# Performance work log

Hardware: AMD Instinct MI355X
Metric: run time of the kernel (lower is better)

## Reference

```python
import jax, jax.numpy as jnp
import numpy as np

B, L, C, H, FF = 2, 2048, 1024, 16, 4096
HD = C // H
SCALE = HD ** -0.5
EPS = 1e-5


def _ln(x, g, b):
    m = jnp.mean(x, axis=-1, keepdims=True)
    v = jnp.mean((x - m) ** 2, axis=-1, keepdims=True)
    return (x - m) * jax.lax.rsqrt(v + EPS) * g + b


def setup_inputs() -> dict:
    key = jax.random.key(0)
    ks = jax.random.split(key, 12)
    s = lambda fan_in: 1.0 / np.sqrt(fan_in)
    return {
        "x": jax.random.normal(ks[0], (B, L, C), jnp.float32),
        "freq_diff": jax.random.normal(ks[1], (B, L), jnp.float32),
        "qkv_w": jax.random.normal(ks[2], (C, 3 * C), jnp.float32) * s(C),
        "qkv_b": jnp.zeros((3 * C,), jnp.float32),
        "fp_w1": jax.random.normal(ks[3], (1, C), jnp.float32),
        "fp_b1": jnp.zeros((C,), jnp.float32),
        "fp_ln_g": jnp.ones((C,), jnp.float32),
        "fp_ln_b": jnp.zeros((C,), jnp.float32),
        "fp_w2": jax.random.normal(ks[4], (C, C), jnp.float32) * s(C),
        "fp_b2": jnp.zeros((C,), jnp.float32),
        "wq_w": jax.random.normal(ks[5], (HD, HD), jnp.float32) * s(HD),
        "wq_b": jnp.zeros((HD,), jnp.float32),
        "wk_w": jax.random.normal(ks[6], (HD, HD), jnp.float32) * s(HD),
        "wk_b": jnp.zeros((HD,), jnp.float32),
        "out_w": jax.random.normal(ks[7], (C, C), jnp.float32) * s(C),
        "out_b": jnp.zeros((C,), jnp.float32),
        "n1_g": jnp.ones((C,), jnp.float32),
        "n1_b": jnp.zeros((C,), jnp.float32),
        "n2_g": jnp.ones((C,), jnp.float32),
        "n2_b": jnp.zeros((C,), jnp.float32),
        "mlp_w1": jax.random.normal(ks[8], (C, FF), jnp.float32) * s(C),
        "mlp_b1": jnp.zeros((FF,), jnp.float32),
        "mlp_w2": jax.random.normal(ks[9], (FF, C), jnp.float32) * s(FF),
        "mlp_b2": jnp.zeros((C,), jnp.float32),
        "freq_scale": jnp.ones((1,), jnp.float32),
    }


def reference(x, freq_diff, qkv_w, qkv_b, fp_w1, fp_b1, fp_ln_g, fp_ln_b,
              fp_w2, fp_b2, wq_w, wq_b, wk_w, wk_b, out_w, out_b,
              n1_g, n1_b, n2_g, n2_b, mlp_w1, mlp_b1, mlp_w2, mlp_b2,
              freq_scale):
    shortcut = x
    xn = _ln(x, n1_g, n1_b)
    qkv = (xn @ qkv_w + qkv_b).reshape(B, L, 3, H, HD)
    qkv = jnp.transpose(qkv, (2, 0, 3, 1, 4))  # [3,B,H,L,HD]
    q, k, v = qkv[0], qkv[1], qkv[2]

    # frequency bias: MLP on scalar freq_diff -> per-head bias vectors
    fb = freq_diff[..., None] @ fp_w1 + fp_b1          # [B,L,C]
    fb = jax.nn.gelu(_ln(fb, fp_ln_g, fp_ln_b), approximate=False)
    fb = fb @ fp_w2 + fp_b2                            # [B,L,C]
    fb = jnp.transpose(fb.reshape(B, L, H, HD), (0, 2, 1, 3))  # [B,H,L,HD]
    qb = fb @ wq_w + wq_b
    kb = fb @ wk_w + wk_b
    freq_attn_bias = jnp.einsum('bhqd,bhkd->bhqk', qb, kb)

    attn = jnp.einsum('bhqd,bhkd->bhqk', q, k) * SCALE
    attn = attn + freq_scale[0] * freq_attn_bias
    attn = jax.nn.softmax(attn, axis=-1)
    o = jnp.einsum('bhqk,bhkd->bhqd', attn, v)
    o = jnp.transpose(o, (0, 2, 1, 3)).reshape(B, L, C)
    x = shortcut + (o @ out_w + out_b)

    xn2 = _ln(x, n2_g, n2_b)
    h = jax.nn.gelu(xn2 @ mlp_w1 + mlp_b1, approximate=False)
    x = x + (h @ mlp_w2 + mlp_b2)
    return x
```

## Files before the change

### kernel.cpp

```cpp
#include <hip/hip_runtime.h>
#include <math.h>


typedef __bf16 bf16;
typedef float f32x4 __attribute__((ext_vector_type(4)));
typedef bf16 bf16x8 __attribute__((ext_vector_type(8)));
typedef bf16 bf16x4 __attribute__((ext_vector_type(4)));

#define DEVINL __device__ __forceinline__

#define LOG2E 1.4426950408889634f

DEVINL float fast_exp2(float x) { return __builtin_amdgcn_exp2f(x); }

DEVINL void async_load16(const void* g, void* l) {
  __builtin_amdgcn_global_load_lds(
      (const __attribute__((address_space(1))) unsigned int*)g,
      (__attribute__((address_space(3))) unsigned int*)l, 16, 0, 0);
}

DEVINL f32x4 mfma16(bf16x8 a, bf16x8 b, f32x4 c) {
  return __builtin_amdgcn_mfma_f32_16x16x32_bf16(a, b, c, 0, 0, 0);
}

DEVINL float gelu_exact(float v) {
  return 0.5f * v * (1.0f + erff(v * 0.70710678118654752f));
}

DEVINL void hard_barrier() {
  asm volatile("" ::: "memory");
  __builtin_amdgcn_s_barrier();
  asm volatile("" ::: "memory");
}

DEVINL void block_reduce2(float& a, float& b, float* red, int tid) {
#pragma unroll
  for (int off = 32; off >= 1; off >>= 1) {
    a += __shfl_xor(a, off);
    b += __shfl_xor(b, off);
  }
  int w = tid >> 6;
  if ((tid & 63) == 0) { red[2 * w] = a; red[2 * w + 1] = b; }
  __syncthreads();
  a = red[0] + red[2] + red[4] + red[6];
  b = red[1] + red[3] + red[5] + red[7];
  __syncthreads();
}

__global__ __launch_bounds__(256) void transpose_cast(
    const float* __restrict__ W, bf16* __restrict__ Wt, int K, int N) {
  __shared__ float tile[32][33];
  int n0 = blockIdx.x * 32, k0 = blockIdx.y * 32;
  int tx = threadIdx.x & 31, ty = threadIdx.x >> 5;
#pragma unroll
  for (int r = 0; r < 4; ++r)
    tile[ty + r * 8][tx] = W[(size_t)(k0 + ty + r * 8) * N + n0 + tx];
  __syncthreads();
#pragma unroll
  for (int r = 0; r < 4; ++r)
    Wt[(size_t)(n0 + ty + r * 8) * K + k0 + tx] = (bf16)tile[tx][ty + r * 8];
}

__global__ __launch_bounds__(256) void prec_qk(
    const float* __restrict__ fp_w2, const float* __restrict__ fp_b2,
    const float* __restrict__ wq_w, const float* __restrict__ wq_b,
    const float* __restrict__ wk_w, const float* __restrict__ wk_b,
    bf16* __restrict__ wqk2t, float* __restrict__ bqk) {
  __shared__ float Wl[64 * 64];
  __shared__ float Al[64 * 128];
  const int id = blockIdx.x;
  const int sel = id >> 7, h = (id >> 3) & 15, ck = id & 7;
  const int t = threadIdx.x;
  const float* wsel = sel ? wk_w : wq_w;
#pragma unroll
  for (int i = 0; i < 4; ++i)
    ((float4*)Wl)[i * 256 + t] = ((const float4*)wsel)[i * 256 + t];
  const int c0 = ck * 128, off = h * 64;
#pragma unroll
  for (int it = 0; it < 8; ++it) {
    int idx = it * 256 + t;
    int rr = idx >> 4, c4 = idx & 15;
    float4 v = *(const float4*)(fp_w2 + (size_t)(c0 + rr) * 1024 + off + c4 * 4);
    float vv[4] = {v.x, v.y, v.z, v.w};
#pragma unroll
    for (int k = 0; k < 4; ++k) {
      int i2 = c4 * 4 + k;
      Al[i2 * 128 + (rr ^ (i2 & 31))] = vv[k];
    }
  }
  __syncthreads();
  const int cr = t & 127, jh = (t >> 7) * 32;
  float acc[32];
#pragma unroll
  for (int j = 0; j < 32; ++j) acc[j] = 0.f;
  for (int i = 0; i < 64; ++i) {
    float a = Al[i * 128 + (cr ^ (i & 31))];
    const float4* wrow = (const float4*)(Wl + i * 64 + jh);
#pragma unroll
    for (int j4 = 0; j4 < 8; ++j4) {
      float4 wv = wrow[j4];
      acc[j4 * 4 + 0] += a * wv.x;
      acc[j4 * 4 + 1] += a * wv.y;
      acc[j4 * 4 + 2] += a * wv.z;
      acc[j4 * 4 + 3] += a * wv.w;
    }
  }
  const int nbase = sel * 1024 + off + jh;
#pragma unroll
  for (int j = 0; j < 32; ++j)
    wqk2t[(size_t)(nbase + j) * 1024 + c0 + cr] = (bf16)acc[j];
  if (ck == 0 && t < 64) {
    float s = 0.f;
    for (int i = 0; i < 64; ++i) s += fp_b2[off + i] * Wl[i * 64 + t];
    bqk[sel * 1024 + off + t] = s + (sel ? wk_b[t] : wq_b[t]);
  }
}

__global__ __launch_bounds__(256) void ln1_kernel(
    const float* __restrict__ x, const float* __restrict__ fd,
    const float* __restrict__ g1, const float* __restrict__ b1,
    const float* __restrict__ fw1, const float* __restrict__ fb1,
    const float* __restrict__ flg, const float* __restrict__ flb,
    bf16* __restrict__ xn, bf16* __restrict__ gout) {
  __shared__ float red[8];
  int tok = blockIdx.x, t = threadIdx.x;
  float4 xv = ((const float4*)(x + (size_t)tok * 1024))[t];
  float s = xv.x + xv.y + xv.z + xv.w;
  float ss = xv.x * xv.x + xv.y * xv.y + xv.z * xv.z + xv.w * xv.w;
  block_reduce2(s, ss, red, t);
  float mean = s * (1.0f / 1024.0f);
  float rsig = rsqrtf(ss * (1.0f / 1024.0f) - mean * mean + 1e-5f);
  float4 g4 = ((const float4*)g1)[t], b4 = ((const float4*)b1)[t];
  bf16x4 o;
  o[0] = (bf16)((xv.x - mean) * rsig * g4.x + b4.x);
  o[1] = (bf16)((xv.y - mean) * rsig * g4.y + b4.y);
  o[2] = (bf16)((xv.z - mean) * rsig * g4.z + b4.z);
  o[3] = (bf16)((xv.w - mean) * rsig * g4.w + b4.w);
  ((bf16x4*)xn)[(size_t)tok * 256 + t] = o;

  float dv = fd[tok];
  float4 w4 = ((const float4*)fw1)[t], c4 = ((const float4*)fb1)[t];
  float f0 = dv * w4.x + c4.x, f1 = dv * w4.y + c4.y;
  float f2 = dv * w4.z + c4.z, f3 = dv * w4.w + c4.w;
  s = f0 + f1 + f2 + f3;
  ss = f0 * f0 + f1 * f1 + f2 * f2 + f3 * f3;
  block_reduce2(s, ss, red, t);
  mean = s * (1.0f / 1024.0f);
  rsig = rsqrtf(ss * (1.0f / 1024.0f) - mean * mean + 1e-5f);
  float4 lg = ((const float4*)flg)[t], lb = ((const float4*)flb)[t];
  bf16x4 q;
  q[0] = (bf16)gelu_exact((f0 - mean) * rsig * lg.x + lb.x);
  q[1] = (bf16)gelu_exact((f1 - mean) * rsig * lg.y + lb.y);
  q[2] = (bf16)gelu_exact((f2 - mean) * rsig * lg.z + lb.z);
  q[3] = (bf16)gelu_exact((f3 - mean) * rsig * lg.w + lb.w);
  ((bf16x4*)gout)[(size_t)tok * 256 + t] = q;
}

__global__ __launch_bounds__(256) void ln_kernel(
    const float* __restrict__ xin, const float* __restrict__ g,
    const float* __restrict__ b, bf16* __restrict__ xout) {
  __shared__ float red[8];
  int tok = blockIdx.x, t = threadIdx.x;
  float4 xv = ((const float4*)(xin + (size_t)tok * 1024))[t];
  float s = xv.x + xv.y + xv.z + xv.w;
  float ss = xv.x * xv.x + xv.y * xv.y + xv.z * xv.z + xv.w * xv.w;
  block_reduce2(s, ss, red, t);
  float mean = s * (1.0f / 1024.0f);
  float rsig = rsqrtf(ss * (1.0f / 1024.0f) - mean * mean + 1e-5f);
  float4 g4 = ((const float4*)g)[t], b4 = ((const float4*)b)[t];
  bf16x4 o;
  o[0] = (bf16)((xv.x - mean) * rsig * g4.x + b4.x);
  o[1] = (bf16)((xv.y - mean) * rsig * g4.y + b4.y);
  o[2] = (bf16)((xv.z - mean) * rsig * g4.z + b4.z);
  o[3] = (bf16)((xv.w - mean) * rsig * g4.w + b4.w);
  ((bf16x4*)xout)[(size_t)tok * 256 + t] = o;
}

#define PHASE(MH, NH, LA, LB, STAGE_STMT, WAIT_STMT)                          \
  do {                                                                        \
    if (LA) {                                                                 \
      _Pragma("unroll") for (int ml = 0; ml < 4; ++ml) {                      \
        _Pragma("unroll") for (int ks = 0; ks < 2; ++ks) {                    \
          const int rr = ml * 16 + lm;                                        \
          const int cc = (((ks * 4 + quad) ^ (lm & 7)) << 3);                 \
          af[ml][ks] = *(const bf16x8*)&As[bsel][MH][wm][rr][cc];             \
        }                                                                     \
      }                                                                       \
    }                                                                         \
    if (LB) {                                                                 \
      _Pragma("unroll") for (int nl = 0; nl < 2; ++nl) {                      \
        _Pragma("unroll") for (int ks = 0; ks < 2; ++ks) {                    \
          const int rr = nl * 16 + lm;                                        \
          const int cc = (((ks * 4 + quad) ^ (lm & 7)) << 3);                 \
          bfr[nl][ks] = *(const bf16x8*)&Bs[bsel][NH][wn][rr][cc];            \
        }                                                                     \
      }                                                                       \
    }                                                                         \
    STAGE_STMT;                                                               \
    hard_barrier();                                                           \
    __builtin_amdgcn_s_setprio(1);                                            \
    _Pragma("unroll") for (int ks = 0; ks < 2; ++ks) {                        \
      _Pragma("unroll") for (int ml = 0; ml < 4; ++ml) {                      \
        _Pragma("unroll") for (int nl = 0; nl < 2; ++nl) {                    \
          acc[(MH)*4 + ml][(NH)*2 + nl] = mfma16(                             \
              af[ml][ks], bfr[nl][ks], acc[(MH)*4 + ml][(NH)*2 + nl]);        \
        }                                                                     \
      }                                                                       \
    }                                                                         \
    __builtin_amdgcn_s_setprio(0);                                            \
    WAIT_STMT;                                                                \
    hard_barrier();                                                           \
  } while (0)

template <class Epi>
__global__ __launch_bounds__(512, 2) void gemm256(
    const bf16* __restrict__ A, const bf16* __restrict__ Bt,
    int lda, int ldb, int K, int kstride, int nbx, int nblk, int rowoffz,
    Epi epi) {
  __shared__ __align__(16) bf16 As[2][2][2][64][64];
  __shared__ __align__(16) bf16 Bs[2][2][4][32][64];

  const int tid = threadIdx.x;
  const int lane = tid & 63, w = tid >> 6;
  const int quad = lane >> 4, lm = lane & 15;
  const int wm = w >> 2, wn = w & 3;

  const int kz = blockIdx.x / nblk;
  const int bid = blockIdx.x - kz * nblk;
  const int swz = (nblk & 7) ? bid : ((bid & 7) * (nblk >> 3) + (bid >> 3));
  const int tm = swz / nbx, tn = swz - tm * nbx;
  const int m0 = tm << 8, n0 = tn << 8;
  const int rowoff = kz * rowoffz;
  A += (size_t)kz * kstride;
  Bt += (size_t)kz * kstride;

  const bf16* Abase = A + (size_t)m0 * lda;
  const bf16* Bbase = Bt + (size_t)n0 * ldb;

  auto stageA = [&](int b, int mh, int kt) {
#pragma unroll
    for (int j = 0; j < 2; ++j) {
      const int q = (w * 2 + j) * 64 + lane;
      const int wm2 = q >> 9, rr = (q >> 3) & 63, c = q & 7;
      async_load16(Abase + (size_t)(wm2 * 128 + mh * 64 + rr) * lda +
                       (size_t)kt * 64 + ((c ^ (rr & 7)) << 3),
                   (char*)&As[b][mh][0][0][0] + (w * 2 + j) * 1024);
    }
  };
  auto stageB = [&](int b, int nh, int kt) {
#pragma unroll
    for (int j = 0; j < 2; ++j) {
      const int q = (w * 2 + j) * 64 + lane;
      const int wn4 = q >> 8, rr = (q >> 3) & 31, c = q & 7;
      async_load16(Bbase + (size_t)(wn4 * 64 + nh * 32 + rr) * ldb +
                       (size_t)kt * 64 + ((c ^ (rr & 7)) << 3),
                   (char*)&Bs[b][nh][0][0][0] + (w * 2 + j) * 1024);
    }
  };

  f32x4 acc[8][4];
#pragma unroll
  for (int i = 0; i < 8; ++i)
#pragma unroll
    for (int j = 0; j < 4; ++j) {
      acc[i][j][0] = 0.f; acc[i][j][1] = 0.f;
      acc[i][j][2] = 0.f; acc[i][j][3] = 0.f;
    }
  bf16x8 af[4][2], bfr[2][2];

  stageA(0, 0, 0);
  stageB(0, 1, 0);
  stageA(0, 1, 0);
  stageB(0, 0, 0);
  stageA(1, 0, 1);
  stageB(1, 1, 1);
  asm volatile("s_waitcnt vmcnt(4)" ::: "memory");
  hard_barrier();

  const int nt = K >> 6;
  int bsel = 0;
  for (int t = 0; t < nt; ++t, bsel ^= 1) {
    PHASE(0, 0, 1, 1, { if (t + 1 < nt) stageA(bsel ^ 1, 1, t + 1); }, {});
    PHASE(0, 1, 0, 1, { if (t + 1 < nt) stageB(bsel ^ 1, 0, t + 1); }, {});
    PHASE(1, 1, 1, 0, { if (t + 2 < nt) stageA(bsel, 0, t + 2); }, {});
    PHASE(1, 0, 0, 1, { if (t + 2 < nt) stageB(bsel, 1, t + 2); },
          {
            if (t + 2 < nt) {
              asm volatile("s_waitcnt vmcnt(4)" ::: "memory");
            } else if (t + 1 < nt) {
              asm volatile("s_waitcnt vmcnt(0)" ::: "memory");
            }
          });
  }

#pragma unroll
  for (int mi = 0; mi < 8; ++mi)
#pragma unroll
    for (int ni = 0; ni < 4; ++ni)
      epi(rowoff + m0 + wm * 128 + mi * 16 + quad * 4,
          n0 + wn * 64 + ni * 16 + lm, acc[mi][ni]);
}

template <class Epi>
__global__ __launch_bounds__(256) void gemm_bf16_k(
    const bf16* __restrict__ A, const bf16* __restrict__ Bt,
    int M, int N, int K, Epi epi) {
  __shared__ bf16 As[2][128 * 32];
  __shared__ bf16 Bs[2][128 * 32];
  const int tid = threadIdx.x;
  const int lane = tid & 63, w = tid >> 6;
  const int quad = lane >> 4, lm = lane & 15;
  const int wm = w >> 1, wn = w & 1;
  const int m0 = blockIdx.y * 128, n0 = blockIdx.x * 128;

  f32x4 acc[4][4];
#pragma unroll
  for (int i = 0; i < 4; ++i)
#pragma unroll
    for (int j = 0; j < 4; ++j) {
      acc[i][j][0] = 0.f; acc[i][j][1] = 0.f; acc[i][j][2] = 0.f; acc[i][j][3] = 0.f;
    }

  const bf16* Ag = A + (size_t)m0 * K;
  const bf16* Bg = Bt + (size_t)n0 * K;

  auto stage = [&](int k0, int buf) {
#pragma unroll
    for (int i = 0; i < 2; ++i) {
      int ch = i * 256 + tid, r = ch >> 2, c = ch & 3;
      async_load16(Ag + (size_t)r * K + k0 + c * 8,
                   (char*)As[buf] + (i * 256 + w * 64) * 16);
      async_load16(Bg + (size_t)r * K + k0 + c * 8,
                   (char*)Bs[buf] + (i * 256 + w * 64) * 16);
    }
  };

  stage(0, 0);
  const int nk = K >> 5;
  for (int ki = 0; ki < nk; ++ki) {
    __syncthreads();
    if (ki + 1 < nk) stage((ki + 1) << 5, (ki + 1) & 1);
    const bf16* Ac = As[ki & 1];
    const bf16* Bc = Bs[ki & 1];
    bf16x8 af[4], bfv[4];
#pragma unroll
    for (int mi = 0; mi < 4; ++mi)
      af[mi] = *(const bf16x8*)(Ac + (wm * 64 + mi * 16 + lm) * 32 + quad * 8);
#pragma unroll
    for (int ni = 0; ni < 4; ++ni)
      bfv[ni] = *(const bf16x8*)(Bc + (wn * 64 + ni * 16 + lm) * 32 + quad * 8);
#pragma unroll
    for (int mi = 0; mi < 4; ++mi)
#pragma unroll
      for (int ni = 0; ni < 4; ++ni)
        acc[mi][ni] = mfma16(af[mi], bfv[ni], acc[mi][ni]);
  }

#pragma unroll
  for (int mi = 0; mi < 4; ++mi)
#pragma unroll
    for (int ni = 0; ni < 4; ++ni)
      epi(m0 + wm * 64 + mi * 16 + quad * 4, n0 + wn * 64 + ni * 16 + lm, acc[mi][ni]);
}

__global__ __launch_bounds__(256) void reduce_mlp2(
    const float* __restrict__ part, float* __restrict__ out) {
  size_t i = (size_t)blockIdx.x * 256 + threadIdx.x;
  const float4* p = (const float4*)part;
  float4 o = ((const float4*)out)[i];
  const size_t S = (size_t)4096 * 256;
  float4 a = p[i], b = p[i + S], c = p[i + 2 * S], d = p[i + 3 * S];
  o.x += a.x + b.x + c.x + d.x;
  o.y += a.y + b.y + c.y + d.y;
  o.z += a.z + b.z + c.z + d.z;
  o.w += a.w + b.w + c.w + d.w;
  ((float4*)out)[i] = o;
}

struct EpiQKV {
  const float* __restrict__ bias;
  bf16 *Qc, *Kc, *Vt;
  DEVINL void operator()(int row, int col, f32x4 v) const {
    int b = row >> 11, l = row & 2047;
    float bia = bias[col];
    if (col < 1024) {
      int h = col >> 6, d = col & 63;
      bf16* p = Qc + (size_t)(((b << 4) + h) * 2048 + l) * 128 + d;
#pragma unroll
      for (int r = 0; r < 4; ++r) p[r * 128] = (bf16)((v[r] + bia) * (0.125f * LOG2E));
    } else if (col < 2048) {
      int c2 = col - 1024, h = c2 >> 6, d = c2 & 63;
      bf16* p = Kc + (size_t)(((b << 4) + h) * 2048 + l) * 128 + d;
#pragma unroll
      for (int r = 0; r < 4; ++r) p[r * 128] = (bf16)(v[r] + bia);
    } else {
      int c2 = col - 2048, h = c2 >> 6, d = c2 & 63;
      bf16x4 pk;
#pragma unroll
      for (int r = 0; r < 4; ++r) pk[r] = (bf16)(v[r] + bia);
      *(bf16x4*)(Vt + (size_t)(((b << 4) + h) * 64 + d) * 2048 + l) = pk;
    }
  }
};

struct EpiQBKB {
  const float* __restrict__ bias;
  const float* __restrict__ fs;
  bf16 *Qc, *Kc;
  DEVINL void operator()(int row, int col, f32x4 v) const {
    int b = row >> 11, l = row & 2047;
    float bia = bias[col];
    if (col < 1024) {
      int h = col >> 6, d = col & 63;
      float sc = fs[0] * LOG2E;
      bf16* p = Qc + (size_t)(((b << 4) + h) * 2048 + l) * 128 + 64 + d;
#pragma unroll
      for (int r = 0; r < 4; ++r) p[r * 128] = (bf16)((v[r] + bia) * sc);
    } else {
      int c2 = col - 1024, h = c2 >> 6, d = c2 & 63;
      bf16* p = Kc + (size_t)(((b << 4) + h) * 2048 + l) * 128 + 64 + d;
#pragma unroll
      for (int r = 0; r < 4; ++r) p[r * 128] = (bf16)(v[r] + bia);
    }
  }
};

struct EpiOut {
  const float* __restrict__ bias;
  const float* __restrict__ x;
  const float* __restrict__ b2;
  float* x1;
  float* out0;
  DEVINL void operator()(int row, int col, f32x4 v) const {
    float bia = bias[col];
    float b2v = b2[col];
#pragma unroll
    for (int r = 0; r < 4; ++r) {
      size_t idx = (size_t)(row + r) * 1024 + col;
      float xv = x[idx] + v[r] + bia;
      x1[idx] = xv;
      out0[idx] = xv + b2v;
    }
  }
};

struct EpiMLP1 {
  const float* __restrict__ bias;
  bf16* hbf;
  DEVINL void operator()(int row, int col, f32x4 v) const {
    float bia = bias[col];
#pragma unroll
    for (int r = 0; r < 4; ++r)
      hbf[(size_t)(row + r) * 4096 + col] = (bf16)gelu_exact(v[r] + bia);
  }
};

struct EpiPart {
  float* part;
  DEVINL void operator()(int row, int col, f32x4 v) const {
#pragma unroll
    for (int r = 0; r < 4; ++r)
      part[(size_t)(row + r) * 1024 + col] = v[r];
  }
};

__global__ __launch_bounds__(512, 4) void flash_kernel(
    const bf16* __restrict__ Qc, const bf16* __restrict__ Kcp,
    const bf16* __restrict__ Vt, bf16* __restrict__ Obf) {
  __shared__ bf16 KsA[64 * 128];
  __shared__ bf16 KsB[64 * 128];
  __shared__ bf16 VsA[64 * 64];
  __shared__ bf16 VsB[64 * 64];
  __shared__ bf16 Ps[128 * 64];

  const int tid = threadIdx.x, lane = tid & 63, w = tid >> 6;
  const int quad = lane >> 4, lm = lane & 15;
  const int id = blockIdx.x;
  const int bh = id & 31, qt = id >> 5;
  const int b = bh >> 4, h = bh & 15;

  const bf16* Qg = Qc + ((size_t)bh * 2048 + qt * 128) * 128;
#pragma unroll
  for (int i = 0; i < 4; ++i) {
    int ch = i * 512 + tid, r = ch >> 4, cs = ch & 15, c = cs ^ (r & 7);
    char* dst = (i < 2) ? (char*)KsA + (i * 512 + w * 64) * 16
                        : (char*)KsB + ((i - 2) * 512 + w * 64) * 16;
    async_load16(Qg + (size_t)r * 128 + c * 8, dst);
  }
  __syncthreads();
  const int qr = w * 16 + lm;
  bf16x8 qf[4];
  {
    const bf16* base = (w < 4) ? KsA : KsB;
    int rr = qr & 63;
#pragma unroll
    for (int ks = 0; ks < 4; ++ks) {
      int pos = (ks * 4 + quad) ^ (lm & 7);
      qf[ks] = *(const bf16x8*)(base + rr * 128 + pos * 8);
    }
  }
  __syncthreads();

  float m_run = -3.0e38f, l_run = 0.f;
  f32x4 o_acc[4];
#pragma unroll
  for (int nf = 0; nf < 4; ++nf) {
    o_acc[nf][0] = 0.f; o_acc[nf][1] = 0.f; o_acc[nf][2] = 0.f; o_acc[nf][3] = 0.f;
  }

  const bf16* Kg0 = Kcp + (size_t)bh * 2048 * 128;
  const bf16* Vg0 = Vt + (size_t)bh * 64 * 2048;

  auto stage = [&](int kv, bf16* Kdst, bf16* Vdst) {
    const bf16* Kg = Kg0 + (size_t)kv * 64 * 128;
#pragma unroll
    for (int i = 0; i < 2; ++i) {
      int ch = i * 512 + tid, key = ch >> 4, c = (ch & 15) ^ (key & 7);
      async_load16(Kg + (size_t)key * 128 + c * 8,
                   (char*)Kdst + (i * 512 + w * 64) * 16);
    }
    {
      int d = tid >> 3, c = (tid & 7) ^ (d & 7);
      async_load16(Vg0 + (size_t)d * 2048 + kv * 64 + c * 8,
                   (char*)Vdst + (w * 64) * 16);
    }
  };

  stage(0, KsA, VsA);

  for (int kv = 0; kv < 32; ++kv) {
    const bf16* Kcur = (kv & 1) ? KsB : KsA;
    const bf16* Vcur = (kv & 1) ? VsB : VsA;
    __syncthreads();
    if (kv + 1 < 32)
      stage(kv + 1, (kv & 1) ? KsA : KsB, (kv & 1) ? VsA : VsB);

    f32x4 sa[4];
#pragma unroll
    for (int nk = 0; nk < 4; ++nk) {
      sa[nk][0] = 0.f; sa[nk][1] = 0.f; sa[nk][2] = 0.f; sa[nk][3] = 0.f;
    }
#pragma unroll
    for (int ks = 0; ks < 4; ++ks) {
      bf16x8 ak[4];
#pragma unroll
      for (int nk = 0; nk < 4; ++nk) {
        int key = nk * 16 + lm;
        int pos = (ks * 4 + quad) ^ (key & 7);
        ak[nk] = *(const bf16x8*)(Kcur + key * 128 + pos * 8);
      }
#pragma unroll
      for (int nk = 0; nk < 4; ++nk)
        sa[nk] = mfma16(ak[nk], qf[ks], sa[nk]);
    }

    float mx = sa[0][0];
#pragma unroll
    for (int nk = 0; nk < 4; ++nk)
#pragma unroll
      for (int rg = 0; rg < 4; ++rg) mx = fmaxf(mx, sa[nk][rg]);
    mx = fmaxf(mx, __shfl_xor(mx, 16));
    mx = fmaxf(mx, __shfl_xor(mx, 32));
    float mnew = fmaxf(m_run, mx);
    float alpha = fast_exp2(m_run - mnew);
    m_run = mnew;
    float rs = 0.f;
#pragma unroll
    for (int nk = 0; nk < 4; ++nk)
#pragma unroll
      for (int rg = 0; rg < 4; ++rg) {
        float pv = fast_exp2(sa[nk][rg] - mnew);
        sa[nk][rg] = pv;
        rs += pv;
      }
    rs += __shfl_xor(rs, 16);
    rs += __shfl_xor(rs, 32);
    l_run = l_run * alpha + rs;
#pragma unroll
    for (int nf = 0; nf < 4; ++nf) {
      o_acc[nf][0] *= alpha; o_acc[nf][1] *= alpha;
      o_acc[nf][2] *= alpha; o_acc[nf][3] *= alpha;
    }

#pragma unroll
    for (int nk = 0; nk < 4; ++nk) {
      int c16 = 2 * nk + (quad >> 1);
      int cs = c16 ^ (lm & 7);
      bf16x4 pk;
      pk[0] = (bf16)sa[nk][0]; pk[1] = (bf16)sa[nk][1];
      pk[2] = (bf16)sa[nk][2]; pk[3] = (bf16)sa[nk][3];
      *(bf16x4*)(Ps + qr * 64 + cs * 8 + (quad & 1) * 4) = pk;
    }

#pragma unroll
    for (int ks = 0; ks < 2; ++ks) {
      bf16x8 pa, vb[4];
      {
        int cs = (ks * 4 + quad) ^ (lm & 7);
        pa = *(const bf16x8*)(Ps + qr * 64 + cs * 8);
      }
#pragma unroll
      for (int nf = 0; nf < 4; ++nf) {
        int d = nf * 16 + lm;
        int cs = (ks * 4 + quad) ^ (d & 7);
        vb[nf] = *(const bf16x8*)(Vcur + d * 64 + cs * 8);
      }
#pragma unroll
      for (int nf = 0; nf < 4; ++nf)
        o_acc[nf] = mfma16(vb[nf], pa, o_acc[nf]);
    }
  }

  float inv = 1.0f / l_run;
  int l = qt * 128 + qr;
#pragma unroll
  for (int nf = 0; nf < 4; ++nf) {
    bf16x4 ov;
#pragma unroll
    for (int rg = 0; rg < 4; ++rg) ov[rg] = (bf16)(o_acc[nf][rg] * inv);
    int d = h * 64 + nf * 16 + quad * 4;
    *(bf16x4*)(Obf + ((size_t)b * 2048 + l) * 1024 + d) = ov;
  }
}

extern "C" void kernel_launch(void* const* d_in, const int* in_sizes, int n_in,
                              void* d_out, int out_size, void* d_ws, size_t ws_size,
                              hipStream_t stream) {
  (void)in_sizes; (void)n_in; (void)out_size; (void)ws_size;
  const float* x      = (const float*)d_in[0];
  const float* fd     = (const float*)d_in[1];
  const float* qkv_w  = (const float*)d_in[2];
  const float* qkv_b  = (const float*)d_in[3];
  const float* fp_w1  = (const float*)d_in[4];
  const float* fp_b1  = (const float*)d_in[5];
  const float* fp_ln_g= (const float*)d_in[6];
  const float* fp_ln_b= (const float*)d_in[7];
  const float* fp_w2  = (const float*)d_in[8];
  const float* fp_b2  = (const float*)d_in[9];
  const float* wq_w   = (const float*)d_in[10];
  const float* wq_b   = (const float*)d_in[11];
  const float* wk_w   = (const float*)d_in[12];
  const float* wk_b   = (const float*)d_in[13];
  const float* out_w  = (const float*)d_in[14];
  const float* out_b  = (const float*)d_in[15];
  const float* n1_g   = (const float*)d_in[16];
  const float* n1_b   = (const float*)d_in[17];
  const float* n2_g   = (const float*)d_in[18];
  const float* n2_b   = (const float*)d_in[19];
  const float* mlp_w1 = (const float*)d_in[20];
  const float* mlp_b1 = (const float*)d_in[21];
  const float* mlp_w2 = (const float*)d_in[22];
  const float* mlp_b2 = (const float*)d_in[23];
  const float* fscale = (const float*)d_in[24];
  float* out = (float*)d_out;

  char* p = (char*)d_ws;
  auto take = [&](size_t n) { char* r = p; p += (n + 255) & ~(size_t)255; return r; };
  bf16* xn_bf  = (bf16*)take((size_t)4096 * 1024 * 2);
  bf16* g_bf   = (bf16*)take((size_t)4096 * 1024 * 2);
  bf16* Qc     = (bf16*)take((size_t)32 * 2048 * 128 * 2);
  bf16* Kc     = (bf16*)take((size_t)32 * 2048 * 128 * 2);
  bf16* Vt     = (bf16*)take((size_t)32 * 64 * 2048 * 2);
  bf16* o_bf   = (bf16*)take((size_t)4096 * 1024 * 2);
  float* x1    = (float*)take((size_t)4096 * 1024 * 4);
  bf16* ln2_bf = (bf16*)take((size_t)4096 * 1024 * 2);
  bf16* h_bf   = (bf16*)take((size_t)4096 * 4096 * 2);
  bf16* qkv_wt = (bf16*)take((size_t)3072 * 1024 * 2);
  bf16* out_wt = (bf16*)take((size_t)1024 * 1024 * 2);
  bf16* w1t    = (bf16*)take((size_t)4096 * 1024 * 2);
  bf16* w2t    = (bf16*)take((size_t)1024 * 4096 * 2);
  bf16* wqk2t  = (bf16*)take((size_t)2048 * 1024 * 2);
  float* bqk   = (float*)take((size_t)2048 * 4);

  float* part = (float*)xn_bf;

  dim3 b256(256), b512(512);

  transpose_cast<<<dim3(3072 / 32, 1024 / 32), b256, 0, stream>>>(qkv_w, qkv_wt, 1024, 3072);
  transpose_cast<<<dim3(1024 / 32, 1024 / 32), b256, 0, stream>>>(out_w, out_wt, 1024, 1024);
  transpose_cast<<<dim3(4096 / 32, 1024 / 32), b256, 0, stream>>>(mlp_w1, w1t, 1024, 4096);
  transpose_cast<<<dim3(1024 / 32, 4096 / 32), b256, 0, stream>>>(mlp_w2, w2t, 4096, 1024);
  prec_qk<<<dim3(256), b256, 0, stream>>>(fp_w2, fp_b2, wq_w, wq_b, wk_w, wk_b, wqk2t, bqk);

  ln1_kernel<<<dim3(4096), b256, 0, stream>>>(x, fd, n1_g, n1_b, fp_w1, fp_b1,
                                              fp_ln_g, fp_ln_b, xn_bf, g_bf);

  gemm256<<<dim3(192), b512, 0, stream>>>(xn_bf, qkv_wt, 1024, 1024, 1024, 0,
                                          12, 192, 0, EpiQKV{qkv_b, Qc, Kc, Vt});
  gemm256<<<dim3(128), b512, 0, stream>>>(g_bf, wqk2t, 1024, 1024, 1024, 0,
                                          8, 128, 0, EpiQBKB{bqk, fscale, Qc, Kc});
  flash_kernel<<<dim3(512), dim3(512), 0, stream>>>(Qc, Kc, Vt, o_bf);

  gemm_bf16_k<<<dim3(8, 32), b256, 0, stream>>>(o_bf, out_wt, 4096, 1024, 1024,
                                                EpiOut{out_b, x, mlp_b2, x1, out});
  ln_kernel<<<dim3(4096), b256, 0, stream>>>(x1, n2_g, n2_b, ln2_bf);
  gemm256<<<dim3(256), b512, 0, stream>>>(ln2_bf, w1t, 1024, 1024, 1024, 0,
                                          16, 256, 0, EpiMLP1{mlp_b1, h_bf});
  gemm256<<<dim3(256), b512, 0, stream>>>(h_bf, w2t, 4096, 4096, 1024, 1024,
                                          4, 64, 4096, EpiPart{part});
  reduce_mlp2<<<dim3(4096), b256, 0, stream>>>(part, out);
}
```

Before: 489.0 us.

## Merge prep kernels, fuse QKV and bias GEMMs, add lazy softmax rescale

Folds the four weight transpose-cast launches and the LN1/frequency-bias kernel into one launch that picks its role from the block index. The QKV GEMM and the frequency-bias QK GEMM now run in a single dual-mode gemm256 launch (320 blocks) with a merged epilogue. In flash attention, the running max and accumulator rescale only when the max grows by more than 8 (log2 units), and the row-sum reduction across lanes is deferred to the end. The aim is to cut launch overhead, fill the GPU better with one larger grid, and remove per-iteration rescale and shuffle work, at the cost of more branching and a bounded loss of exp range.

```diff
diff --git a/kernel.cpp b/kernel.cpp
--- a/kernel.cpp
+++ b/kernel.cpp
@@ -47,83 +47,45 @@
   __syncthreads();
 }
 
-__global__ __launch_bounds__(256) void transpose_cast(
-    const float* __restrict__ W, bf16* __restrict__ Wt, int K, int N) {
-  __shared__ float tile[32][33];
-  int n0 = blockIdx.x * 32, k0 = blockIdx.y * 32;
-  int tx = threadIdx.x & 31, ty = threadIdx.x >> 5;
-#pragma unroll
-  for (int r = 0; r < 4; ++r)
-    tile[ty + r * 8][tx] = W[(size_t)(k0 + ty + r * 8) * N + n0 + tx];
-  __syncthreads();
-#pragma unroll
-  for (int r = 0; r < 4; ++r)
-    Wt[(size_t)(n0 + ty + r * 8) * K + k0 + tx] = (bf16)tile[tx][ty + r * 8];
-}
-
-__global__ __launch_bounds__(256) void prec_qk(
-    const float* __restrict__ fp_w2, const float* __restrict__ fp_b2,
-    const float* __restrict__ wq_w, const float* __restrict__ wq_b,
-    const float* __restrict__ wk_w, const float* __restrict__ wk_b,
-    bf16* __restrict__ wqk2t, float* __restrict__ bqk) {
-  __shared__ float Wl[64 * 64];
-  __shared__ float Al[64 * 128];
-  const int id = blockIdx.x;
-  const int sel = id >> 7, h = (id >> 3) & 15, ck = id & 7;
-  const int t = threadIdx.x;
-  const float* wsel = sel ? wk_w : wq_w;
-#pragma unroll
-  for (int i = 0; i < 4; ++i)
-    ((float4*)Wl)[i * 256 + t] = ((const float4*)wsel)[i * 256 + t];
-  const int c0 = ck * 128, off = h * 64;
-#pragma unroll
-  for (int it = 0; it < 8; ++it) {
-    int idx = it * 256 + t;
-    int rr = idx >> 4, c4 = idx & 15;
-    float4 v = *(const float4*)(fp_w2 + (size_t)(c0 + rr) * 1024 + off + c4 * 4);
-    float vv[4] = {v.x, v.y, v.z, v.w};
-#pragma unroll
-    for (int k = 0; k < 4; ++k) {
-      int i2 = c4 * 4 + k;
-      Al[i2 * 128 + (rr ^ (i2 & 31))] = vv[k];
-    }
-  }
-  __syncthreads();
-  const int cr = t & 127, jh = (t >> 7) * 32;
-  float acc[32];
-#pragma unroll
-  for (int j = 0; j < 32; ++j) acc[j] = 0.f;
-  for (int i = 0; i < 64; ++i) {
-    float a = Al[i * 128 + (cr ^ (i & 31))];
-    const float4* wrow = (const float4*)(Wl + i * 64 + jh);
-#pragma unroll
-    for (int j4 = 0; j4 < 8; ++j4) {
-      float4 wv = wrow[j4];
-      acc[j4 * 4 + 0] += a * wv.x;
-      acc[j4 * 4 + 1] += a * wv.y;
-      acc[j4 * 4 + 2] += a * wv.z;
-      acc[j4 * 4 + 3] += a * wv.w;
-    }
-  }
-  const int nbase = sel * 1024 + off + jh;
-#pragma unroll
-  for (int j = 0; j < 32; ++j)
-    wqk2t[(size_t)(nbase + j) * 1024 + c0 + cr] = (bf16)acc[j];
-  if (ck == 0 && t < 64) {
-    float s = 0.f;
-    for (int i = 0; i < 64; ++i) s += fp_b2[off + i] * Wl[i * 64 + t];
-    bqk[sel * 1024 + off + t] = s + (sel ? wk_b[t] : wq_b[t]);
-  }
-}
-
-__global__ __launch_bounds__(256) void ln1_kernel(
+__global__ __launch_bounds__(256) void pre_kernel(
+    const float* __restrict__ qkv_w, const float* __restrict__ out_w,
+    const float* __restrict__ mlp_w1, const float* __restrict__ mlp_w2,
+    bf16* __restrict__ qkv_wt, bf16* __restrict__ out_wt,
+    bf16* __restrict__ w1t, bf16* __restrict__ w2t,
     const float* __restrict__ x, const float* __restrict__ fd,
     const float* __restrict__ g1, const float* __restrict__ b1,
     const float* __restrict__ fw1, const float* __restrict__ fb1,
     const float* __restrict__ flg, const float* __restrict__ flb,
     bf16* __restrict__ xn, bf16* __restrict__ gout) {
+  __shared__ float tile[32][33];
   __shared__ float red[8];
-  int tok = blockIdx.x, t = threadIdx.x;
+  const int id = blockIdx.x, t = threadIdx.x;
+  if (id < 12288) {
+    const float* W; bf16* Wt; int K, N, bx, by;
+    if (id < 3072) {
+      W = qkv_w; Wt = qkv_wt; K = 1024; N = 3072; bx = id % 96; by = id / 96;
+    } else if (id < 4096) {
+      int i = id - 3072;
+      W = out_w; Wt = out_wt; K = 1024; N = 1024; bx = i & 31; by = i >> 5;
+    } else if (id < 8192) {
+      int i = id - 4096;
+      W = mlp_w1; Wt = w1t; K = 1024; N = 4096; bx = i & 127; by = i >> 7;
+    } else {
+      int i = id - 8192;
+      W = mlp_w2; Wt = w2t; K = 4096; N = 1024; bx = i & 31; by = i >> 5;
+    }
+    int n0 = bx * 32, k0 = by * 32;
+    int tx = t & 31, ty = t >> 5;
+#pragma unroll
+    for (int r = 0; r < 4; ++r)
+      tile[ty + r * 8][tx] = W[(size_t)(k0 + ty + r * 8) * N + n0 + tx];
+    __syncthreads();
+#pragma unroll
+    for (int r = 0; r < 4; ++r)
+      Wt[(size_t)(n0 + ty + r * 8) * K + k0 + tx] = (bf16)tile[tx][ty + r * 8];
+    return;
+  }
+  int tok = id - 12288;
   float4 xv = ((const float4*)(x + (size_t)tok * 1024))[t];
   float s = xv.x + xv.y + xv.z + xv.w;
   float ss = xv.x * xv.x + xv.y * xv.y + xv.z * xv.z + xv.w * xv.w;
@@ -154,6 +116,61 @@
   q[2] = (bf16)gelu_exact((f2 - mean) * rsig * lg.z + lb.z);
   q[3] = (bf16)gelu_exact((f3 - mean) * rsig * lg.w + lb.w);
   ((bf16x4*)gout)[(size_t)tok * 256 + t] = q;
+}
+
+__global__ __launch_bounds__(256) void prec_qk(
+    const float* __restrict__ fp_w2, const float* __restrict__ fp_b2,
+    const float* __restrict__ wq_w, const float* __restrict__ wq_b,
+    const float* __restrict__ wk_w, const float* __restrict__ wk_b,
+    bf16* __restrict__ wqk2t, float* __restrict__ bqk) {
+  __shared__ float Wl[64 * 64];
+  __shared__ float Al[64 * 128];
+  const int id = blockIdx.x;
+  const int sel = id >> 7, h = (id >> 3) & 15, ck = id & 7;
+  const int t = threadIdx.x;
+  const float* wsel = sel ? wk_w : wq_w;
+#pragma unroll
+  for (int i = 0; i < 4; ++i)
+    ((float4*)Wl)[i * 256 + t] = ((const float4*)wsel)[i * 256 + t];
+  const int c0 = ck * 128, off = h * 64;
+#pragma unroll
+  for (int it = 0; it < 8; ++it) {
+    int idx = it * 256 + t;
+    int rr = idx >> 4, c4 = idx & 15;
+    float4 v = *(const float4*)(fp_w2 + (size_t)(c0 + rr) * 1024 + off + c4 * 4);
+    float vv[4] = {v.x, v.y, v.z, v.w};
+#pragma unroll
+    for (int k = 0; k < 4; ++k) {
+      int i2 = c4 * 4 + k;
+      Al[i2 * 128 + (rr ^ (i2 & 31))] = vv[k];
+    }
+  }
+  __syncthreads();
+  const int cr = t & 127, jh = (t >> 7) * 32;
+  float acc[32];
+#pragma unroll
+  for (int j = 0; j < 32; ++j) acc[j] = 0.f;
+  for (int i = 0; i < 64; ++i) {
+    float a = Al[i * 128 + (cr ^ (i & 31))];
+    const float4* wrow = (const float4*)(Wl + i * 64 + jh);
+#pragma unroll
+    for (int j4 = 0; j4 < 8; ++j4) {
+      float4 wv = wrow[j4];
+      acc[j4 * 4 + 0] += a * wv.x;
+      acc[j4 * 4 + 1] += a * wv.y;
+      acc[j4 * 4 + 2] += a * wv.z;
+      acc[j4 * 4 + 3] += a * wv.w;
+    }
+  }
+  const int nbase = sel * 1024 + off + jh;
+#pragma unroll
+  for (int j = 0; j < 32; ++j)
+    wqk2t[(size_t)(nbase + j) * 1024 + c0 + cr] = (bf16)acc[j];
+  if (ck == 0 && t < 64) {
+    float s = 0.f;
+    for (int i = 0; i < 64; ++i) s += fp_b2[off + i] * Wl[i * 64 + t];
+    bqk[sel * 1024 + off + t] = s + (sel ? wk_b[t] : wq_b[t]);
+  }
 }
 
 __global__ __launch_bounds__(256) void ln_kernel(
@@ -212,11 +229,12 @@
     hard_barrier();                                                           \
   } while (0)
 
-template <class Epi>
+template <bool DUAL, class Epi>
 __global__ __launch_bounds__(512, 2) void gemm256(
     const bf16* __restrict__ A, const bf16* __restrict__ Bt,
+    const bf16* __restrict__ A2, const bf16* __restrict__ Bt2,
     int lda, int ldb, int K, int kstride, int nbx, int nblk, int rowoffz,
-    Epi epi) {
+    int nblk1, int nbx2, Epi epi) {
   __shared__ __align__(16) bf16 As[2][2][2][64][64];
   __shared__ __align__(16) bf16 Bs[2][2][4][32][64];
 
@@ -226,16 +244,23 @@
   const int wm = w >> 2, wn = w & 3;
 
   const int kz = blockIdx.x / nblk;
-  const int bid = blockIdx.x - kz * nblk;
-  const int swz = (nblk & 7) ? bid : ((bid & 7) * (nblk >> 3) + (bid >> 3));
-  const int tm = swz / nbx, tn = swz - tm * nbx;
+  int bid = blockIdx.x - kz * nblk;
+  int mode = 0, nbx_ = nbx, nb_ = DUAL ? nblk1 : nblk;
+  const bf16* Ap = A;
+  const bf16* Bp = Bt;
+  if (DUAL && bid >= nblk1) {
+    mode = 1; bid -= nblk1; nbx_ = nbx2; nb_ = nblk - nblk1;
+    Ap = A2; Bp = Bt2;
+  }
+  const int swz = (nb_ & 7) ? bid : ((bid & 7) * (nb_ >> 3) + (bid >> 3));
+  const int tm = swz / nbx_, tn = swz - tm * nbx_;
   const int m0 = tm << 8, n0 = tn << 8;
   const int rowoff = kz * rowoffz;
-  A += (size_t)kz * kstride;
-  Bt += (size_t)kz * kstride;
-
-  const bf16* Abase = A + (size_t)m0 * lda;
-  const bf16* Bbase = Bt + (size_t)n0 * ldb;
+  Ap += (size_t)kz * kstride;
+  Bp += (size_t)kz * kstride;
+
+  const bf16* Abase = Ap + (size_t)m0 * lda;
+  const bf16* Bbase = Bp + (size_t)n0 * ldb;
 
   auto stageA = [&](int b, int mh, int kt) {
 #pragma unroll
@@ -297,7 +322,7 @@
   for (int mi = 0; mi < 8; ++mi)
 #pragma unroll
     for (int ni = 0; ni < 4; ++ni)
-      epi(rowoff + m0 + wm * 128 + mi * 16 + quad * 4,
+      epi(mode, rowoff + m0 + wm * 128 + mi * 16 + quad * 4,
           n0 + wn * 64 + ni * 16 + lm, acc[mi][ni]);
 }
 
@@ -377,50 +402,46 @@
   ((float4*)out)[i] = o;
 }
 
-struct EpiQKV {
-  const float* __restrict__ bias;
+struct EpiFused {
+  const float* __restrict__ qkvb;
+  const float* __restrict__ bqk;
+  const float* __restrict__ fs;
   bf16 *Qc, *Kc, *Vt;
-  DEVINL void operator()(int row, int col, f32x4 v) const {
+  DEVINL void operator()(int mode, int row, int col, f32x4 v) const {
     int b = row >> 11, l = row & 2047;
-    float bia = bias[col];
-    if (col < 1024) {
-      int h = col >> 6, d = col & 63;
-      bf16* p = Qc + (size_t)(((b << 4) + h) * 2048 + l) * 128 + d;
-#pragma unroll
-      for (int r = 0; r < 4; ++r) p[r * 128] = (bf16)((v[r] + bia) * (0.125f * LOG2E));
-    } else if (col < 2048) {
-      int c2 = col - 1024, h = c2 >> 6, d = c2 & 63;
-      bf16* p = Kc + (size_t)(((b << 4) + h) * 2048 + l) * 128 + d;
-#pragma unroll
-      for (int r = 0; r < 4; ++r) p[r * 128] = (bf16)(v[r] + bia);
+    if (mode == 0) {
+      float bia = qkvb[col];
+      if (col < 1024) {
+        int h = col >> 6, d = col & 63;
+        bf16* p = Qc + (size_t)(((b << 4) + h) * 2048 + l) * 128 + d;
+#pragma unroll
+        for (int r = 0; r < 4; ++r) p[r * 128] = (bf16)((v[r] + bia) * (0.125f * LOG2E));
+      } else if (col < 2048) {
+        int c2 = col - 1024, h = c2 >> 6, d = c2 & 63;
+        bf16* p = Kc + (size_t)(((b << 4) + h) * 2048 + l) * 128 + d;
+#pragma unroll
+        for (int r = 0; r < 4; ++r) p[r * 128] = (bf16)(v[r] + bia);
+      } else {
+        int c2 = col - 2048, h = c2 >> 6, d = c2 & 63;
+        bf16x4 pk;
+#pragma unroll
+        for (int r = 0; r < 4; ++r) pk[r] = (bf16)(v[r] + bia);
+        *(bf16x4*)(Vt + (size_t)(((b << 4) + h) * 64 + d) * 2048 + l) = pk;
+      }
     } else {
-      int c2 = col - 2048, h = c2 >> 6, d = c2 & 63;
-      bf16x4 pk;
-#pragma unroll
-      for (int r = 0; r < 4; ++r) pk[r] = (bf16)(v[r] + bia);
-      *(bf16x4*)(Vt + (size_t)(((b << 4) + h) * 64 + d) * 2048 + l) = pk;
-    }
-  }
-};
-
-struct EpiQBKB {
-  const float* __restrict__ bias;
-  const float* __restrict__ fs;
-  bf16 *Qc, *Kc;
-  DEVINL void operator()(int row, int col, f32x4 v) const {
-    int b = row >> 11, l = row & 2047;
-    float bia = bias[col];
-    if (col < 1024) {
-      int h = col >> 6, d = col & 63;
-      float sc = fs[0] * LOG2E;
-      bf16* p = Qc + (size_t)(((b << 4) + h) * 2048 + l) * 128 + 64 + d;
-#pragma unroll
-      for (int r = 0; r < 4; ++r) p[r * 128] = (bf16)((v[r] + bia) * sc);
-    } else {
-      int c2 = col - 1024, h = c2 >> 6, d = c2 & 63;
-      bf16* p = Kc + (size_t)(((b << 4) + h) * 2048 + l) * 128 + 64 + d;
-#pragma unroll
-      for (int r = 0; r < 4; ++r) p[r * 128] = (bf16)(v[r] + bia);
+      float bia = bqk[col];
+      if (col < 1024) {
+        int h = col >> 6, d = col & 63;
+        float sc = fs[0] * LOG2E;
+        bf16* p = Qc + (size_t)(((b << 4) + h) * 2048 + l) * 128 + 64 + d;
+#pragma unroll
+        for (int r = 0; r < 4; ++r) p[r * 128] = (bf16)((v[r] + bia) * sc);
+      } else {
+        int c2 = col - 1024, h = c2 >> 6, d = c2 & 63;
+        bf16* p = Kc + (size_t)(((b << 4) + h) * 2048 + l) * 128 + 64 + d;
+#pragma unroll
+        for (int r = 0; r < 4; ++r) p[r * 128] = (bf16)(v[r] + bia);
+      }
     }
   }
 };
@@ -447,7 +468,7 @@
 struct EpiMLP1 {
   const float* __restrict__ bias;
   bf16* hbf;
-  DEVINL void operator()(int row, int col, f32x4 v) const {
+  DEVINL void operator()(int, int row, int col, f32x4 v) const {
     float bia = bias[col];
 #pragma unroll
     for (int r = 0; r < 4; ++r)
@@ -457,7 +478,7 @@
 
 struct EpiPart {
   float* part;
-  DEVINL void operator()(int row, int col, f32x4 v) const {
+  DEVINL void operator()(int, int row, int col, f32x4 v) const {
 #pragma unroll
     for (int r = 0; r < 4; ++r)
       part[(size_t)(row + r) * 1024 + col] = v[r];
@@ -501,7 +522,7 @@
   }
   __syncthreads();
 
-  float m_run = -3.0e38f, l_run = 0.f;
+  float m_run = -3.0e38f, l_lane = 0.f;
   f32x4 o_acc[4];
 #pragma unroll
   for (int nf = 0; nf < 4; ++nf) {
@@ -554,33 +575,37 @@
         sa[nk] = mfma16(ak[nk], qf[ks], sa[nk]);
     }
 
-    float mx = sa[0][0];
-#pragma unroll
-    for (int nk = 0; nk < 4; ++nk)
-#pragma unroll
-      for (int rg = 0; rg < 4; ++rg) mx = fmaxf(mx, sa[nk][rg]);
+    float mx = fmaxf(fmaxf(sa[0][0], sa[0][1]), sa[0][2]);
+    mx = fmaxf(fmaxf(mx, sa[0][3]), sa[1][0]);
+    mx = fmaxf(fmaxf(mx, sa[1][1]), sa[1][2]);
+    mx = fmaxf(fmaxf(mx, sa[1][3]), sa[2][0]);
+    mx = fmaxf(fmaxf(mx, sa[2][1]), sa[2][2]);
+    mx = fmaxf(fmaxf(mx, sa[2][3]), sa[3][0]);
+    mx = fmaxf(fmaxf(mx, sa[3][1]), sa[3][2]);
+    mx = fmaxf(mx, sa[3][3]);
     mx = fmaxf(mx, __shfl_xor(mx, 16));
     mx = fmaxf(mx, __shfl_xor(mx, 32));
-    float mnew = fmaxf(m_run, mx);
-    float alpha = fast_exp2(m_run - mnew);
-    m_run = mnew;
+    if (__any(mx > m_run + 8.0f)) {
+      float mnew = fmaxf(m_run, mx);
+      float alpha = fast_exp2(m_run - mnew);
+      m_run = mnew;
+      l_lane *= alpha;
+#pragma unroll
+      for (int nf = 0; nf < 4; ++nf) {
+        o_acc[nf][0] *= alpha; o_acc[nf][1] *= alpha;
+        o_acc[nf][2] *= alpha; o_acc[nf][3] *= alpha;
+      }
+    }
     float rs = 0.f;
 #pragma unroll
     for (int nk = 0; nk < 4; ++nk)
 #pragma unroll
       for (int rg = 0; rg < 4; ++rg) {
-        float pv = fast_exp2(sa[nk][rg] - mnew);
+        float pv = fast_exp2(sa[nk][rg] - m_run);
         sa[nk][rg] = pv;
         rs += pv;
       }
-    rs += __shfl_xor(rs, 16);
-    rs += __shfl_xor(rs, 32);
-    l_run = l_run * alpha + rs;
-#pragma unroll
-    for (int nf = 0; nf < 4; ++nf) {
-      o_acc[nf][0] *= alpha; o_acc[nf][1] *= alpha;
-      o_acc[nf][2] *= alpha; o_acc[nf][3] *= alpha;
-    }
+    l_lane += rs;
 
 #pragma unroll
     for (int nk = 0; nk < 4; ++nk) {
@@ -611,7 +636,10 @@
     }
   }
 
-  float inv = 1.0f / l_run;
+  float lt = l_lane;
+  lt += __shfl_xor(lt, 16);
+  lt += __shfl_xor(lt, 32);
+  float inv = 1.0f / lt;
   int l = qt * 128 + qr;
 #pragma unroll
   for (int nf = 0; nf < 4; ++nf) {
@@ -676,27 +704,24 @@
 
   dim3 b256(256), b512(512);
 
-  transpose_cast<<<dim3(3072 / 32, 1024 / 32), b256, 0, stream>>>(qkv_w, qkv_wt, 1024, 3072);
-  transpose_cast<<<dim3(1024 / 32, 1024 / 32), b256, 0, stream>>>(out_w, out_wt, 1024, 1024);
-  transpose_cast<<<dim3(4096 / 32, 1024 / 32), b256, 0, stream>>>(mlp_w1, w1t, 1024, 4096);
-  transpose_cast<<<dim3(1024 / 32, 4096 / 32), b256, 0, stream>>>(mlp_w2, w2t, 4096, 1024);
   prec_qk<<<dim3(256), b256, 0, stream>>>(fp_w2, fp_b2, wq_w, wq_b, wk_w, wk_b, wqk2t, bqk);
-
-  ln1_kernel<<<dim3(4096), b256, 0, stream>>>(x, fd, n1_g, n1_b, fp_w1, fp_b1,
-                                              fp_ln_g, fp_ln_b, xn_bf, g_bf);
-
-  gemm256<<<dim3(192), b512, 0, stream>>>(xn_bf, qkv_wt, 1024, 1024, 1024, 0,
-                                          12, 192, 0, EpiQKV{qkv_b, Qc, Kc, Vt});
-  gemm256<<<dim3(128), b512, 0, stream>>>(g_bf, wqk2t, 1024, 1024, 1024, 0,
-                                          8, 128, 0, EpiQBKB{bqk, fscale, Qc, Kc});
+  pre_kernel<<<dim3(16384), b256, 0, stream>>>(
+      qkv_w, out_w, mlp_w1, mlp_w2, qkv_wt, out_wt, w1t, w2t,
+      x, fd, n1_g, n1_b, fp_w1, fp_b1, fp_ln_g, fp_ln_b, xn_bf, g_bf);
+
+  gemm256<true><<<dim3(320), b512, 0, stream>>>(
+      xn_bf, qkv_wt, g_bf, wqk2t, 1024, 1024, 1024, 0,
+      12, 320, 0, 192, 8, EpiFused{qkv_b, bqk, fscale, Qc, Kc, Vt});
   flash_kernel<<<dim3(512), dim3(512), 0, stream>>>(Qc, Kc, Vt, o_bf);
 
   gemm_bf16_k<<<dim3(8, 32), b256, 0, stream>>>(o_bf, out_wt, 4096, 1024, 1024,
                                                 EpiOut{out_b, x, mlp_b2, x1, out});
   ln_kernel<<<dim3(4096), b256, 0, stream>>>(x1, n2_g, n2_b, ln2_bf);
-  gemm256<<<dim3(256), b512, 0, stream>>>(ln2_bf, w1t, 1024, 1024, 1024, 0,
-                                          16, 256, 0, EpiMLP1{mlp_b1, h_bf});
-  gemm256<<<dim3(256), b512, 0, stream>>>(h_bf, w2t, 4096, 4096, 1024, 1024,
-                                          4, 64, 4096, EpiPart{part});
+  gemm256<false><<<dim3(256), b512, 0, stream>>>(
+      ln2_bf, w1t, nullptr, nullptr, 1024, 1024, 1024, 0,
+      16, 256, 0, 0, 0, EpiMLP1{mlp_b1, h_bf});
+  gemm256<false><<<dim3(256), b512, 0, stream>>>(
+      h_bf, w2t, nullptr, nullptr, 4096, 4096, 1024, 1024,
+      4, 64, 4096, 0, 0, EpiPart{part});
   reduce_mlp2<<<dim3(4096), b256, 0, stream>>>(part, out);
 }
```

Result: slower. 607.7 us (+24.3%).
